# Performance work log

Hardware: AMD Instinct MI355X
Metric: run time of the kernel (lower is better)

Reference implementation:

```python
import jax, jax.numpy as jnp
import numpy as np

B, S, D, H = 4, 4096, 1024, 16
DK = D // H
EPS = 1e-6

def _feature_map(x):
    # ELU + 1 -> strictly positive features
    return jax.nn.elu(x) + 1.0

def setup_inputs() -> dict:
    key = jax.random.key(0)
    ks = jax.random.split(key, 11)
    s = 1.0 / np.sqrt(D)
    return {
        "query": jax.random.normal(ks[0], (B, S, D), jnp.float32),
        "key":   jax.random.normal(ks[1], (B, S, D), jnp.float32),
        "value": jax.random.normal(ks[2], (B, S, D), jnp.float32),
        "Wq": jax.random.uniform(ks[3], (D, D), jnp.float32, -s, s),
        "bq": jax.random.uniform(ks[4], (D,), jnp.float32, -s, s),
        "Wk": jax.random.uniform(ks[5], (D, D), jnp.float32, -s, s),
        "bk": jax.random.uniform(ks[6], (D,), jnp.float32, -s, s),
        "Wv": jax.random.uniform(ks[7], (D, D), jnp.float32, -s, s),
        "bv": jax.random.uniform(ks[8], (D,), jnp.float32, -s, s),
        "Wo": jax.random.uniform(ks[9], (D, D), jnp.float32, -s, s),
        "bo": jax.random.uniform(ks[10], (D,), jnp.float32, -s, s),
    }

def reference(query, key, value, Wq, bq, Wk, bk, Wv, bv, Wo, bo):
    def heads(x, W, b):
        # torch Linear: x @ W.T + b, then split heads -> [B, H, S, DK]
        y = x @ W.T + b
        return y.reshape(B, S, H, DK).transpose(0, 2, 1, 3)

    Q = _feature_map(heads(query, Wq, bq))
    K = _feature_map(heads(key, Wk, bk))
    V = heads(value, Wv, bv)

    # KV[b,h,m,d] = sum_n K[b,h,n,d] * V[b,h,n,m]  (d: K feat dim, m: V dim)
    KV = jnp.einsum('bhnd,bhnm->bhmd', K, V)
    # normalizer Z[b,h,n] = Q[b,h,n,:] . sum_n K
    Z = jnp.einsum('bhnd,bhd->bhn', Q, K.sum(axis=2))[..., None] + EPS
    out = jnp.einsum('bhnd,bhmd->bhnm', Q, KV) / Z  # [B,H,S,DK]
    out = out.transpose(0, 2, 1, 3).reshape(B, S, D)
    return out @ Wo.T + bo
```

## Files before the change

### kernel.cpp

```cpp
#include <hip/hip_runtime.h>
#include <math.h>

#define Bb 4
#define Ss 4096
#define Dd 1024
#define Hh 16
#define DKk 64
#define Mm (Bb * Ss)
#define NCH 16

typedef __attribute__((ext_vector_type(8))) short bf16x8;
typedef __attribute__((ext_vector_type(4))) float f32x4;

__device__ __forceinline__ unsigned short f2bf(float f) {
  unsigned u = __float_as_uint(f);
  u += 0x7FFFu + ((u >> 16) & 1u);
  return (unsigned short)(u >> 16);
}
__device__ __forceinline__ float bf2f(unsigned short s) {
  return __uint_as_float(((unsigned)s) << 16);
}

#define GLOAD(dst, src)                                                     \
  __builtin_amdgcn_global_load_lds(                                         \
      (const __attribute__((address_space(1))) void*)(src),                 \
      (__attribute__((address_space(3))) void*)(dst), 16, 0, 0)

__global__ __launch_bounds__(256) void cvt_f32_bf16(
    const float* __restrict__ s0, const float* __restrict__ s1,
    const float* __restrict__ s2, const float* __restrict__ s3,
    unsigned short* __restrict__ d0, unsigned short* __restrict__ d1,
    unsigned short* __restrict__ d2, unsigned short* __restrict__ d3, int n4) {
  const float* s; unsigned short* d;
  switch (blockIdx.y) {
    case 0:  s = s0; d = d0; break;
    case 1:  s = s1; d = d1; break;
    case 2:  s = s2; d = d2; break;
    default: s = s3; d = d3; break;
  }
  const int i = blockIdx.x * 256 + threadIdx.x;
  if (i < n4) {
    float4 v = ((const float4*)s)[i];
    ushort4 o;
    o.x = f2bf(v.x); o.y = f2bf(v.y); o.z = f2bf(v.z); o.w = f2bf(v.w);
    ((ushort4*)d)[i] = o;
  }
}

#define PHASE(mh, nh)                                                        \
  {                                                                          \
    bf16x8 af[4][2], bv_[2][2];                                              \
    _Pragma("unroll") for (int mi = 0; mi < 4; ++mi)                         \
      _Pragma("unroll") for (int ks = 0; ks < 2; ++ks)                       \
        af[mi][ks] = *(const bf16x8*)(bufA +                                 \
            (rowA0 + (mh) * 64 + mi * 16) * 64 + (swz_rd ^ (ks * 32)));      \
    _Pragma("unroll") for (int ni = 0; ni < 2; ++ni)                         \
      _Pragma("unroll") for (int ks = 0; ks < 2; ++ks)                       \
        bv_[ni][ks] = *(const bf16x8*)(bufB +                                \
            (rowB0 + (nh) * 32 + ni * 16) * 64 + (swz_rd ^ (ks * 32)));      \
    __builtin_amdgcn_s_setprio(1);                                           \
    _Pragma("unroll") for (int mi = 0; mi < 4; ++mi)                         \
      _Pragma("unroll") for (int ni = 0; ni < 2; ++ni)                       \
        _Pragma("unroll") for (int ks = 0; ks < 2; ++ks)                     \
          acc[(mh) * 4 + mi][(nh) * 2 + ni] =                                \
              __builtin_amdgcn_mfma_f32_16x16x32_bf16(                       \
                  af[mi][ks], bv_[ni][ks],                                   \
                  acc[(mh) * 4 + mi][(nh) * 2 + ni], 0, 0, 0);               \
    __builtin_amdgcn_s_setprio(0);                                           \
  }

template <int ACT, typename OutT>
__global__ __launch_bounds__(512, 2) void gemm256(
    const unsigned short* __restrict__ A,
    const unsigned short* __restrict__ W,
    const float* __restrict__ bias,
    OutT* __restrict__ C) {
  __shared__ __align__(16) unsigned short lds[2 * 32768];
  const int t = threadIdx.x;
  const int wave = t >> 6, lane = t & 63;
  const int wm = wave >> 2, wn = wave & 3;
  const int fr = lane & 15, fq = lane >> 4;

  int wg = blockIdx.x + gridDim.x * blockIdx.y;
  wg = ((wg & 7) << 5) | (wg >> 3);
  const int bm = wg >> 2, bn = wg & 3;

  f32x4 acc[8][4];
#pragma unroll
  for (int i = 0; i < 8; ++i)
#pragma unroll
    for (int j = 0; j < 4; ++j) acc[i][j] = (f32x4){0.f, 0.f, 0.f, 0.f};

  const int rbase = t >> 3;
  const int swz_st = ((t & 7) ^ ((t >> 3) & 7)) << 3;
  const unsigned short* gA[4];
  const unsigned short* gB[4];
#pragma unroll
  for (int l = 0; l < 4; ++l) {
    const int r = l * 64 + rbase;
    gA[l] = A + (size_t)(bm * 256 + r) * Dd + swz_st;
    gB[l] = W + (size_t)(bn * 256 + r) * Dd + swz_st;
  }
  const int dstoff = wave * 512;

  const int rowA0 = wm * 128 + fr;
  const int rowB0 = wn * 64 + fr;
  const int swz_rd = (fq * 8) ^ ((fr & 7) << 3);

#pragma unroll
  for (int l = 0; l < 4; ++l) {
    GLOAD(lds + l * 4096 + dstoff, gA[l]);
    GLOAD(lds + 16384 + l * 4096 + dstoff, gB[l]);
  }

  for (int tt = 0; tt < 16; ++tt) {
    unsigned short* bufA = lds + (tt & 1) * 32768;
    unsigned short* bufB = bufA + 16384;
    unsigned short* nA = lds + ((tt & 1) ^ 1) * 32768;
    unsigned short* nB = nA + 16384;
    const int kpre = (tt < 15 ? tt + 1 : 15) * 64;

#pragma unroll
    for (int l = 0; l < 4; ++l) GLOAD(nA + l * 4096 + dstoff, gA[l] + kpre);
    asm volatile("s_waitcnt vmcnt(4)" ::: "memory");
    __builtin_amdgcn_s_barrier();
    PHASE(0, 0)
    __builtin_amdgcn_s_barrier();
#pragma unroll
    for (int l = 0; l < 4; ++l) GLOAD(nB + l * 4096 + dstoff, gB[l] + kpre);
    PHASE(0, 1)
    __builtin_amdgcn_s_barrier();
    PHASE(1, 0)
    __builtin_amdgcn_s_barrier();
    PHASE(1, 1)
    __builtin_amdgcn_s_barrier();
  }

  const size_t row0 = (size_t)bm * 256 + wm * 128 + fq * 4;
  const int col0 = bn * 256 + wn * 64 + fr;
#pragma unroll
  for (int mi = 0; mi < 8; ++mi) {
#pragma unroll
    for (int ni = 0; ni < 4; ++ni) {
      const int col = col0 + ni * 16;
      const float bvl = bias[col];
#pragma unroll
      for (int r = 0; r < 4; ++r) {
        const size_t row = row0 + mi * 16 + r;
        float vv = acc[mi][ni][r] + bvl;
        if (ACT) vv = (vv > 0.f) ? (vv + 1.f) : __expf(vv);
        if constexpr (sizeof(OutT) == 2)
          ((unsigned short*)C)[row * Dd + col] = f2bf(vv);
        else
          ((float*)C)[row * Dd + col] = vv;
      }
    }
  }
}

__global__ __launch_bounds__(256) void kv_partial(
    const unsigned short* __restrict__ Kf, const unsigned short* __restrict__ Vf,
    float* __restrict__ part) {
  const int bx = blockIdx.x;
  const int chunk = bx % NCH;
  const int bh = bx / NCH;
  const int h = bh % Hh, b = bh / Hh;
  const int t = threadIdx.x;
  const int tm = t >> 4, td = t & 15;
  __shared__ float sK[8][64];
  __shared__ float sV[8][64];
  float acc[4][4] = {{0.f}};
  float ksr[4] = {0.f, 0.f, 0.f, 0.f};

  const int which = t >> 7;
  const int idx = t & 127;
  const int rr = idx >> 4;
  const int dpos = (idx & 15) << 2;
  const int colbase = h * DKk;
  const int rows = Ss / NCH;

  for (int n0 = 0; n0 < rows; n0 += 8) {
    const int gr = b * Ss + chunk * rows + n0 + rr;
    const unsigned short* src = which ? Vf : Kf;
    ushort4 raw = *(const ushort4*)&src[(size_t)gr * Dd + colbase + dpos];
    __syncthreads();
    float* dst = which ? &sV[rr][dpos] : &sK[rr][dpos];
    dst[0] = bf2f(raw.x); dst[1] = bf2f(raw.y);
    dst[2] = bf2f(raw.z); dst[3] = bf2f(raw.w);
    __syncthreads();
#pragma unroll
    for (int r = 0; r < 8; ++r) {
      float kv[4], vv[4];
#pragma unroll
      for (int j = 0; j < 4; ++j) kv[j] = sK[r][td * 4 + j];
#pragma unroll
      for (int i = 0; i < 4; ++i) vv[i] = sV[r][tm * 4 + i];
#pragma unroll
      for (int i = 0; i < 4; ++i)
#pragma unroll
        for (int j = 0; j < 4; ++j)
          acc[i][j] = fmaf(vv[i], kv[j], acc[i][j]);
      if (tm == 0) {
#pragma unroll
        for (int j = 0; j < 4; ++j) ksr[j] += kv[j];
      }
    }
  }

  float* p = part + (size_t)bx * 4160;
#pragma unroll
  for (int i = 0; i < 4; ++i)
#pragma unroll
    for (int j = 0; j < 4; ++j)
      p[(tm * 4 + i) * 64 + td * 4 + j] = acc[i][j];
  if (tm == 0) {
#pragma unroll
    for (int j = 0; j < 4; ++j) p[4096 + td * 4 + j] = ksr[j];
  }
}

__global__ __launch_bounds__(256) void kv_reduce(
    const float* __restrict__ part, float* __restrict__ KV,
    float* __restrict__ Ksum) {
  const int bh = blockIdx.x;
  for (int e = threadIdx.x; e < 4160; e += 256) {
    float s = 0.f;
#pragma unroll
    for (int c = 0; c < NCH; ++c)
      s += part[((size_t)bh * NCH + c) * 4160 + e];
    if (e < 4096) KV[(size_t)bh * 4096 + e] = s;
    else Ksum[bh * 64 + (e - 4096)] = s;
  }
}

__global__ __launch_bounds__(256) void attn_mfma(
    unsigned short* __restrict__ Qf, const float* __restrict__ KV,
    const float* __restrict__ Ksum) {
  const int bh = blockIdx.x;
  const int h = bh & (Hh - 1), b = bh >> 4;
  const int t = threadIdx.x;
  const int wave = t >> 6, lane = t & 63;
  const int fr = lane & 15, fq = lane >> 4;

  bf16x8 bfrag[4][2];
  const float* kvb = KV + (size_t)bh * 4096;
#pragma unroll
  for (int nj = 0; nj < 4; ++nj)
#pragma unroll
    for (int ks = 0; ks < 2; ++ks) {
      const float* src = kvb + (nj * 16 + fr) * 64 + ks * 32 + fq * 8;
      const float4 lo = *(const float4*)src;
      const float4 hi = *(const float4*)(src + 4);
      bf16x8 f;
      f[0] = (short)f2bf(lo.x); f[1] = (short)f2bf(lo.y);
      f[2] = (short)f2bf(lo.z); f[3] = (short)f2bf(lo.w);
      f[4] = (short)f2bf(hi.x); f[5] = (short)f2bf(hi.y);
      f[6] = (short)f2bf(hi.z); f[7] = (short)f2bf(hi.w);
      bfrag[nj][ks] = f;
    }
  bf16x8 zfrag[2];
#pragma unroll
  for (int ks = 0; ks < 2; ++ks) {
    bf16x8 f = (bf16x8){0, 0, 0, 0, 0, 0, 0, 0};
    if (fr == 0) {
      const float* src = Ksum + bh * 64 + ks * 32 + fq * 8;
      const float4 lo = *(const float4*)src;
      const float4 hi = *(const float4*)(src + 4);
      f[0] = (short)f2bf(lo.x); f[1] = (short)f2bf(lo.y);
      f[2] = (short)f2bf(lo.z); f[3] = (short)f2bf(lo.w);
      f[4] = (short)f2bf(hi.x); f[5] = (short)f2bf(hi.y);
      f[6] = (short)f2bf(hi.z); f[7] = (short)f2bf(hi.w);
    }
    zfrag[ks] = f;
  }

  const size_t row0 = (size_t)b * Ss + (size_t)blockIdx.y * 256 + wave * 64;
  unsigned short* qbase = Qf + row0 * Dd + h * DKk;
  bf16x8 afrag[4][2];
#pragma unroll
  for (int mi = 0; mi < 4; ++mi)
#pragma unroll
    for (int ks = 0; ks < 2; ++ks)
      afrag[mi][ks] =
          *(const bf16x8*)(qbase + (size_t)(mi * 16 + fr) * Dd + ks * 32 + fq * 8);

  f32x4 acc[4][4], zacc[4];
#pragma unroll
  for (int mi = 0; mi < 4; ++mi) {
    zacc[mi] = (f32x4){0.f, 0.f, 0.f, 0.f};
#pragma unroll
    for (int nj = 0; nj < 4; ++nj) acc[mi][nj] = (f32x4){0.f, 0.f, 0.f, 0.f};
  }
#pragma unroll
  for (int mi = 0; mi < 4; ++mi)
#pragma unroll
    for (int ks = 0; ks < 2; ++ks) {
      zacc[mi] = __builtin_amdgcn_mfma_f32_16x16x32_bf16(
          afrag[mi][ks], zfrag[ks], zacc[mi], 0, 0, 0);
#pragma unroll
      for (int nj = 0; nj < 4; ++nj)
        acc[mi][nj] = __builtin_amdgcn_mfma_f32_16x16x32_bf16(
            afrag[mi][ks], bfrag[nj][ks], acc[mi][nj], 0, 0, 0);
    }

#pragma unroll
  for (int mi = 0; mi < 4; ++mi)
#pragma unroll
    for (int r = 0; r < 4; ++r) {
      const float zv = __shfl(zacc[mi][r], lane & 48) + 1e-6f;
      const float rz = 1.0f / zv;
      const size_t ro = (size_t)(mi * 16 + fq * 4 + r) * Dd;
#pragma unroll
      for (int nj = 0; nj < 4; ++nj)
        qbase[ro + nj * 16 + fr] = f2bf(acc[mi][nj][r] * rz);
    }
}

extern "C" void kernel_launch(void* const* d_in, const int* in_sizes, int n_in,
                              void* d_out, int out_size, void* d_ws, size_t ws_size,
                              hipStream_t stream) {
  const float* q  = (const float*)d_in[0];
  const float* k  = (const float*)d_in[1];
  const float* v  = (const float*)d_in[2];
  const float* Wq = (const float*)d_in[3];
  const float* bq = (const float*)d_in[4];
  const float* Wk = (const float*)d_in[5];
  const float* bk = (const float*)d_in[6];
  const float* Wv = (const float*)d_in[7];
  const float* bv = (const float*)d_in[8];
  const float* Wo = (const float*)d_in[9];
  const float* bo = (const float*)d_in[10];
  float* out = (float*)d_out;

  unsigned short* cb0 = (unsigned short*)d_ws;
  unsigned short* cb1 = cb0 + (size_t)Mm * Dd;
  unsigned short* Kf  = cb1 + (size_t)Mm * Dd;
  unsigned short* Vf  = Kf  + (size_t)Mm * Dd;
  unsigned short* Wqb = Vf  + (size_t)Mm * Dd;
  unsigned short* Wkb = Wqb + (size_t)Dd * Dd;
  unsigned short* Wvb = Wkb + (size_t)Dd * Dd;
  unsigned short* Wob = Wvb + (size_t)Dd * Dd;
  float* KV   = (float*)(Wob + (size_t)Dd * Dd);
  float* Ksum = KV + (size_t)Bb * Hh * DKk * DKk;
  float* part = (float*)cb1;

  dim3 gg(Dd / 256, Mm / 256);

  cvt_f32_bf16<<<dim3(1024, 4), 256, 0, stream>>>(Wq, Wk, Wv, Wo, Wqb, Wkb, Wvb, Wob,
                                                  (Dd * Dd) / 4);
  cvt_f32_bf16<<<dim3(16384, 2), 256, 0, stream>>>(k, v, nullptr, nullptr,
                                                   cb0, cb1, nullptr, nullptr,
                                                   ((size_t)Mm * Dd) / 4);
  gemm256<1, unsigned short><<<gg, 512, 0, stream>>>(cb0, Wkb, bk, Kf);
  gemm256<0, unsigned short><<<gg, 512, 0, stream>>>(cb1, Wvb, bv, Vf);
  kv_partial<<<Bb * Hh * NCH, 256, 0, stream>>>(Kf, Vf, part);
  kv_reduce<<<Bb * Hh, 256, 0, stream>>>(part, KV, Ksum);
  cvt_f32_bf16<<<dim3(16384, 1), 256, 0, stream>>>(q, nullptr, nullptr, nullptr,
                                                   cb0, nullptr, nullptr, nullptr,
                                                   ((size_t)Mm * Dd) / 4);
  gemm256<1, unsigned short><<<gg, 512, 0, stream>>>(cb0, Wqb, bq, Kf);
  attn_mfma<<<dim3(Bb * Hh, Ss / 256), 256, 0, stream>>>(Kf, KV, Ksum);
  gemm256<0, float><<<gg, 512, 0, stream>>>(Kf, Wob, bo, out);
}
```

Before: 295.6 us.

## Fuse fp32-to-bf16 activation conversion into GEMM A-tile loading

The GEMM now reads fp32 activations directly into registers, converts them to bf16 with packed convert instructions, and writes them to LDS, replacing separate conversion kernels for q, k and v. This removes three full passes that wrote and reread the large bf16 activation copies, and drops the workspace buffers they used. The cost is that A tiles now take a register path instead of async global-to-LDS loads. That adds register pressure and VALU work inside the pipelined loop, and the B prefetch is moved earlier.

New measurement: 295.2 us. About the same (-0.1%).

```diff
diff --git a/kernel.cpp b/kernel.cpp
--- a/kernel.cpp
+++ b/kernel.cpp
@@ -19,6 +19,11 @@
 }
 __device__ __forceinline__ float bf2f(unsigned short s) {
   return __uint_as_float(((unsigned)s) << 16);
+}
+__device__ __forceinline__ unsigned cvt2(float lo, float hi) {
+  unsigned r;
+  asm("v_cvt_pk_bf16_f32 %0, %1, %2" : "=v"(r) : "v"(lo), "v"(hi));
+  return r;
 }
 
 #define GLOAD(dst, src)                                                     \
@@ -69,12 +74,13 @@
     __builtin_amdgcn_s_setprio(0);                                           \
   }
 
-template <int ACT, typename OutT>
+template <int ACT, typename AT, typename OutT>
 __global__ __launch_bounds__(512, 2) void gemm256(
-    const unsigned short* __restrict__ A,
+    const AT* __restrict__ A,
     const unsigned short* __restrict__ W,
     const float* __restrict__ bias,
     OutT* __restrict__ C) {
+  constexpr bool AF32 = (sizeof(AT) == 4);
   __shared__ __align__(16) unsigned short lds[2 * 32768];
   const int t = threadIdx.x;
   const int wave = t >> 6, lane = t & 63;
@@ -93,13 +99,19 @@
 
   const int rbase = t >> 3;
   const int swz_st = ((t & 7) ^ ((t >> 3) & 7)) << 3;
-  const unsigned short* gA[4];
   const unsigned short* gB[4];
+  const AT* gAf[4];
+  int wrA[4];
 #pragma unroll
   for (int l = 0; l < 4; ++l) {
     const int r = l * 64 + rbase;
-    gA[l] = A + (size_t)(bm * 256 + r) * Dd + swz_st;
     gB[l] = W + (size_t)(bn * 256 + r) * Dd + swz_st;
+    if constexpr (AF32) {
+      gAf[l] = A + (size_t)(bm * 256 + r) * Dd + ((t & 7) << 3);
+      wrA[l] = r * 64 + swz_st;
+    } else {
+      gAf[l] = A + (size_t)(bm * 256 + r) * Dd + swz_st;
+    }
   }
   const int dstoff = wave * 512;
 
@@ -107,10 +119,31 @@
   const int rowB0 = wn * 64 + fr;
   const int swz_rd = (fq * 8) ^ ((fr & 7) << 3);
 
-#pragma unroll
-  for (int l = 0; l < 4; ++l) {
-    GLOAD(lds + l * 4096 + dstoff, gA[l]);
-    GLOAD(lds + 16384 + l * 4096 + dstoff, gB[l]);
+  if constexpr (AF32) {
+    float4 p0[4], p1[4];
+#pragma unroll
+    for (int l = 0; l < 4; ++l) {
+      p0[l] = *(const float4*)(gAf[l]);
+      p1[l] = *(const float4*)(gAf[l] + 4);
+    }
+#pragma unroll
+    for (int l = 0; l < 4; ++l) GLOAD(lds + 16384 + l * 4096 + dstoff, gB[l]);
+    asm volatile("s_waitcnt vmcnt(4)" ::: "memory");
+#pragma unroll
+    for (int l = 0; l < 4; ++l) {
+      int4 w;
+      w.x = cvt2(p0[l].x, p0[l].y); w.y = cvt2(p0[l].z, p0[l].w);
+      w.z = cvt2(p1[l].x, p1[l].y); w.w = cvt2(p1[l].z, p1[l].w);
+      *(int4*)(lds + wrA[l]) = w;
+    }
+    asm volatile("s_waitcnt lgkmcnt(0)" ::: "memory");
+    __builtin_amdgcn_sched_barrier(0);
+  } else {
+#pragma unroll
+    for (int l = 0; l < 4; ++l) {
+      GLOAD(lds + l * 4096 + dstoff, gAf[l]);
+      GLOAD(lds + 16384 + l * 4096 + dstoff, gB[l]);
+    }
   }
 
   for (int tt = 0; tt < 16; ++tt) {
@@ -120,19 +153,44 @@
     unsigned short* nB = nA + 16384;
     const int kpre = (tt < 15 ? tt + 1 : 15) * 64;
 
-#pragma unroll
-    for (int l = 0; l < 4; ++l) GLOAD(nA + l * 4096 + dstoff, gA[l] + kpre);
-    asm volatile("s_waitcnt vmcnt(4)" ::: "memory");
+    float4 a0[4], a1[4];
+    if constexpr (AF32) {
+#pragma unroll
+      for (int l = 0; l < 4; ++l) {
+        a0[l] = *(const float4*)(gAf[l] + kpre);
+        a1[l] = *(const float4*)(gAf[l] + kpre + 4);
+      }
+#pragma unroll
+      for (int l = 0; l < 4; ++l) GLOAD(nB + l * 4096 + dstoff, gB[l] + kpre);
+      asm volatile("s_waitcnt vmcnt(12)" ::: "memory");
+    } else {
+#pragma unroll
+      for (int l = 0; l < 4; ++l) {
+        GLOAD(nA + l * 4096 + dstoff, gAf[l] + kpre);
+        GLOAD(nB + l * 4096 + dstoff, gB[l] + kpre);
+      }
+      asm volatile("s_waitcnt vmcnt(8)" ::: "memory");
+    }
     __builtin_amdgcn_s_barrier();
     PHASE(0, 0)
     __builtin_amdgcn_s_barrier();
-#pragma unroll
-    for (int l = 0; l < 4; ++l) GLOAD(nB + l * 4096 + dstoff, gB[l] + kpre);
     PHASE(0, 1)
     __builtin_amdgcn_s_barrier();
     PHASE(1, 0)
     __builtin_amdgcn_s_barrier();
     PHASE(1, 1)
+    if constexpr (AF32) {
+      asm volatile("s_waitcnt vmcnt(4)" ::: "memory");
+#pragma unroll
+      for (int l = 0; l < 4; ++l) {
+        int4 w;
+        w.x = cvt2(a0[l].x, a0[l].y); w.y = cvt2(a0[l].z, a0[l].w);
+        w.z = cvt2(a1[l].x, a1[l].y); w.w = cvt2(a1[l].z, a1[l].w);
+        *(int4*)(nA + wrA[l]) = w;
+      }
+      asm volatile("s_waitcnt lgkmcnt(0)" ::: "memory");
+      __builtin_amdgcn_sched_barrier(0);
+    }
     __builtin_amdgcn_s_barrier();
   }
 
@@ -332,9 +390,7 @@
   const float* bo = (const float*)d_in[10];
   float* out = (float*)d_out;
 
-  unsigned short* cb0 = (unsigned short*)d_ws;
-  unsigned short* cb1 = cb0 + (size_t)Mm * Dd;
-  unsigned short* Kf  = cb1 + (size_t)Mm * Dd;
+  unsigned short* Kf  = (unsigned short*)d_ws;
   unsigned short* Vf  = Kf  + (size_t)Mm * Dd;
   unsigned short* Wqb = Vf  + (size_t)Mm * Dd;
   unsigned short* Wkb = Wqb + (size_t)Dd * Dd;
@@ -342,23 +398,17 @@
   unsigned short* Wob = Wvb + (size_t)Dd * Dd;
   float* KV   = (float*)(Wob + (size_t)Dd * Dd);
   float* Ksum = KV + (size_t)Bb * Hh * DKk * DKk;
-  float* part = (float*)cb1;
+  float* part = Ksum + Bb * Hh * DKk;
 
   dim3 gg(Dd / 256, Mm / 256);
 
   cvt_f32_bf16<<<dim3(1024, 4), 256, 0, stream>>>(Wq, Wk, Wv, Wo, Wqb, Wkb, Wvb, Wob,
                                                   (Dd * Dd) / 4);
-  cvt_f32_bf16<<<dim3(16384, 2), 256, 0, stream>>>(k, v, nullptr, nullptr,
-                                                   cb0, cb1, nullptr, nullptr,
-                                                   ((size_t)Mm * Dd) / 4);
-  gemm256<1, unsigned short><<<gg, 512, 0, stream>>>(cb0, Wkb, bk, Kf);
-  gemm256<0, unsigned short><<<gg, 512, 0, stream>>>(cb1, Wvb, bv, Vf);
+  gemm256<1, float, unsigned short><<<gg, 512, 0, stream>>>(k, Wkb, bk, Kf);
+  gemm256<0, float, unsigned short><<<gg, 512, 0, stream>>>(v, Wvb, bv, Vf);
   kv_partial<<<Bb * Hh * NCH, 256, 0, stream>>>(Kf, Vf, part);
   kv_reduce<<<Bb * Hh, 256, 0, stream>>>(part, KV, Ksum);
-  cvt_f32_bf16<<<dim3(16384, 1), 256, 0, stream>>>(q, nullptr, nullptr, nullptr,
-                                                   cb0, nullptr, nullptr, nullptr,
-                                                   ((size_t)Mm * Dd) / 4);
-  gemm256<1, unsigned short><<<gg, 512, 0, stream>>>(cb0, Wqb, bq, Kf);
+  gemm256<1, float, unsigned short><<<gg, 512, 0, stream>>>(q, Wqb, bq, Kf);
   attn_mfma<<<dim3(Bb * Hh, Ss / 256), 256, 0, stream>>>(Kf, KV, Ksum);
-  gemm256<0, float><<<gg, 512, 0, stream>>>(Kf, Wob, bo, out);
-}
+  gemm256<0, unsigned short, float><<<gg, 512, 0, stream>>>(Kf, Wob, bo, out);
+}
```
